# Kernel tuning notes

Measured on AMD Instinct MI355X. Metric: run time of the kernel, lower is better.

Reference implementation:

```python
import jax, jax.numpy as jnp
import numpy as np

TOPK_RATIO = 0.2
DICE_WEIGHT = 0.5
SHAPE = (2, 1, 128, 192, 192)


def setup_inputs() -> dict:
    key = jax.random.key(0)
    k1, k2 = jax.random.split(key)
    logits = jax.random.normal(k1, SHAPE, dtype=jnp.float32)
    targets = jax.random.uniform(k2, SHAPE, dtype=jnp.float32)
    return {"logits": logits, "targets": targets}


def _bce_with_logits(x, t):
    # stable: max(x,0) - x*t + log(1+exp(-|x|))
    return jnp.maximum(x, 0.0) - x * t + jnp.log1p(jnp.exp(-jnp.abs(x)))


def reference(logits, targets):
    # --- TopK BCE ---
    flat_loss = _bce_with_logits(logits, targets).reshape(-1)
    n = flat_loss.shape[0]
    k_samples = max(1, int(n * TOPK_RATIO))
    topk_losses, _ = jax.lax.top_k(flat_loss, k_samples)
    bce = jnp.mean(topk_losses)

    # --- Soft Dice ---
    p = jax.nn.sigmoid(logits).reshape(-1)
    t = targets.reshape(-1)
    intersection = jnp.sum(p * t)
    union = jnp.sum(p) + jnp.sum(t)
    dice = (2.0 * intersection + 1e-06) / (union + 1e-06)
    dice_loss = 1.0 - dice

    return bce + DICE_WEIGHT * dice_loss
```

## Files before the change

### kernel.cpp

```cpp
#include <hip/hip_runtime.h>
#include <math.h>
#include <limits.h>

#define NB1 8192
#define NB2 4096
#define VEC 4
#define NREP 4

__device__ unsigned g_H1[NB1];
__device__ unsigned g_hist2[NREP * NB2];
__device__ float    g_band[2];
__device__ unsigned g_done1 = 0;

__device__ __forceinline__ void elem_f(float x, float t, float& l, float& p) {
    float e = __expf(-fabsf(x));
    l = fmaxf(x, 0.f) - x * t + __logf(1.f + e);
    float r = __builtin_amdgcn_rcpf(1.f + e);
    p = (x >= 0.f) ? r : e * r;
}

__global__ __launch_bounds__(256) void sample_band_kernel(
    const float4* __restrict__ x4, const float4* __restrict__ t4,
    int n4, long long ks, long long M)
{
    __shared__ unsigned lh[NB1];
    __shared__ int is_last;
    for (int i = threadIdx.x; i < NB1; i += 256) lh[i] = 0u;
    __syncthreads();

    int nth = gridDim.x * 256;
    int tid = blockIdx.x * 256 + threadIdx.x;
    int S4 = n4 >> 4;
    int i0 = tid, i1 = tid + nth;

    float4 xa, ta, xb, tb;
    bool v0 = i0 < S4, v1 = i1 < S4;
    if (v0) {
        int f4 = ((i0 >> 6) << 10) + (i0 & 63);
        xa = x4[f4]; ta = t4[f4];
    }
    if (v1) {
        int f4 = ((i1 >> 6) << 10) + (i1 & 63);
        xb = x4[f4]; tb = t4[f4];
    }
    if (v0) {
        float xs[4] = {xa.x, xa.y, xa.z, xa.w};
        float ts[4] = {ta.x, ta.y, ta.z, ta.w};
        #pragma unroll
        for (int c = 0; c < 4; ++c) {
            float l, p; elem_f(xs[c], ts[c], l, p);
            atomicAdd(&lh[__float_as_uint(l) >> 19], 1u);
        }
    }
    if (v1) {
        float xs[4] = {xb.x, xb.y, xb.z, xb.w};
        float ts[4] = {tb.x, tb.y, tb.z, tb.w};
        #pragma unroll
        for (int c = 0; c < 4; ++c) {
            float l, p; elem_f(xs[c], ts[c], l, p);
            atomicAdd(&lh[__float_as_uint(l) >> 19], 1u);
        }
    }
    __syncthreads();
    for (int i = threadIdx.x; i < NB1; i += 256) {
        unsigned c = lh[i];
        if (c) atomicAdd(&g_H1[i], c);
    }
    __syncthreads();

    if (threadIdx.x == 0) {
        __threadfence();
        is_last = (atomicAdd(&g_done1, 1u) == (unsigned)(gridDim.x - 1));
    }
    __syncthreads();
    if (!is_last) return;
    __threadfence();

    const uint4* hv = (const uint4*)g_H1;
    uint4* lv = (uint4*)lh;
    for (int i = threadIdx.x; i < NB1 / 4; i += 256) lv[i] = hv[i];
    __syncthreads();
    for (int i = threadIdx.x; i < NB1; i += 256) g_H1[i] = 0u;
    if (threadIdx.x == 0) g_done1 = 0u;

    if (threadIdx.x < 64) {
        int lane = threadIdx.x;
        int base = lane << 7;
        unsigned long long chunk = 0;
        for (int j = 0; j < 128; ++j) chunk += lh[base + j];
        unsigned long long s = chunk;
        #pragma unroll
        for (int off = 1; off < 64; off <<= 1) {
            unsigned long long v = __shfl_down(s, off);
            if (lane + off < 64) s += v;
        }
        unsigned long long above = s - chunk;

        int my_bhi = INT_MAX, my_blo = -1;
        unsigned long long c = above;
        for (int j = 127; j >= 0; --j) {
            unsigned h = lh[base + j];
            if ((long long)(c + h) < ks - M) my_bhi = base + j;
            if ((long long)c > ks + M && my_blo < 0) my_blo = base + j;
            c += h;
        }
        #pragma unroll
        for (int off = 32; off; off >>= 1) {
            int a = __shfl_down(my_bhi, off); my_bhi = min(my_bhi, a);
            int b = __shfl_down(my_blo, off); my_blo = max(my_blo, b);
        }
        if (lane == 0) {
            int bhi = (my_bhi == INT_MAX) ? (NB1 - 1) : my_bhi;
            int blo = my_blo;
            float vhi = __uint_as_float((unsigned)bhi << 19);
            float vlo = (blo < 0) ? 0.f : __uint_as_float((unsigned)(blo + 1) << 19);
            if (!(vlo < vhi)) vlo = 0.f;
            g_band[0] = vlo;
            g_band[1] = vhi;
        }
    }
}

__device__ __forceinline__ void process4(
    float4 xv, float4 tv, float vlo, float vhi, float scale,
    float& sp, float& spt, float& st, float& sgt, unsigned& cnt,
    unsigned (&lhist)[NB2])
{
    float xs[4] = {xv.x, xv.y, xv.z, xv.w};
    float ts[4] = {tv.x, tv.y, tv.z, tv.w};
    #pragma unroll
    for (int c = 0; c < 4; ++c) {
        float l, p;
        elem_f(xs[c], ts[c], l, p);
        sp += p; spt += p * ts[c]; st += ts[c];
        if (l >= vhi) { cnt++; sgt += l; }
        else if (l >= vlo) {
            int b = min((int)((l - vlo) * scale), NB2 - 1);
            atomicAdd(&lhist[b], 1u);
        }
    }
}

__global__ __launch_bounds__(256, 4) void main_kernel(
    const float4* __restrict__ x4, const float4* __restrict__ t4,
    float* __restrict__ q0, float* __restrict__ q1,
    float* __restrict__ q2, float* __restrict__ q3, unsigned* __restrict__ qc,
    const float* __restrict__ xg, const float* __restrict__ tg,
    int n, int n4)
{
    __shared__ unsigned lhist[NB2];
    for (int i = threadIdx.x; i < NB2; i += 256) lhist[i] = 0u;
    __syncthreads();

    float vlo = g_band[0], vhi = g_band[1];
    float scale = (float)NB2 / (vhi - vlo);

    int base = blockIdx.x * (256 * VEC) + threadIdx.x;
    float sp = 0.f, spt = 0.f, st = 0.f, sgt = 0.f;
    unsigned cnt = 0;

    bool full = (blockIdx.x + 1) * (256 * VEC) <= n4;
    if (full) {
        float4 xv[VEC], tv[VEC];
        #pragma unroll
        for (int j = 0; j < VEC; ++j) xv[j] = x4[base + j * 256];
        #pragma unroll
        for (int j = 0; j < VEC; ++j) tv[j] = t4[base + j * 256];
        #pragma unroll
        for (int j = 0; j < VEC; ++j)
            process4(xv[j], tv[j], vlo, vhi, scale, sp, spt, st, sgt, cnt, lhist);
    } else {
        for (int j = 0; j < VEC; ++j) {
            int idx = base + j * 256;
            if (idx < n4)
                process4(x4[idx], t4[idx], vlo, vhi, scale, sp, spt, st, sgt, cnt, lhist);
        }
    }
    int tail0 = n4 << 2;
    if (blockIdx.x == 0 && threadIdx.x < (n - tail0)) {
        float x = xg[tail0 + threadIdx.x], t = tg[tail0 + threadIdx.x];
        float l, p;
        elem_f(x, t, l, p);
        sp += p; spt += p * t; st += t;
        if (l >= vhi) { cnt++; sgt += l; }
        else if (l >= vlo) {
            int b = min((int)((l - vlo) * scale), NB2 - 1);
            atomicAdd(&lhist[b], 1u);
        }
    }

    __syncthreads();
    {
        unsigned* dst = &g_hist2[(blockIdx.x & (NREP - 1)) * NB2];
        for (int i = threadIdx.x; i < NB2; i += 256) {
            unsigned c = lhist[i];
            if (c) atomicAdd(&dst[i], c);
        }
    }

    #pragma unroll
    for (int off = 32; off; off >>= 1) {
        sp  += __shfl_down(sp,  off);
        spt += __shfl_down(spt, off);
        st  += __shfl_down(st,  off);
        sgt += __shfl_down(sgt, off);
        cnt += __shfl_down(cnt, off);
    }
    __shared__ float    rs[4][4];
    __shared__ unsigned rc[4];
    int w = threadIdx.x >> 6;
    if ((threadIdx.x & 63) == 0) {
        rs[w][0] = sp; rs[w][1] = spt; rs[w][2] = st; rs[w][3] = sgt; rc[w] = cnt;
    }
    __syncthreads();
    if (threadIdx.x == 0) {
        float a0 = 0, a1 = 0, a2 = 0, a3 = 0;
        unsigned c = 0;
        #pragma unroll
        for (int i = 0; i < 4; ++i) {
            a0 += rs[i][0]; a1 += rs[i][1]; a2 += rs[i][2]; a3 += rs[i][3]; c += rc[i];
        }
        q0[blockIdx.x] = a0; q1[blockIdx.x] = a1; q2[blockIdx.x] = a2;
        q3[blockIdx.x] = a3; qc[blockIdx.x] = c;
    }
}

__global__ __launch_bounds__(1024) void final_kernel(
    const float* __restrict__ q0, const float* __restrict__ q1,
    const float* __restrict__ q2, const float* __restrict__ q3,
    const unsigned* __restrict__ qc, int nblocks,
    float* __restrict__ out, long long k)
{
    __shared__ unsigned lh[NB2];
    __shared__ double red[16][5];
    __shared__ double fin[5];

    for (int i = threadIdx.x; i < NB2; i += 1024) {
        unsigned s = 0;
        #pragma unroll
        for (int r = 0; r < NREP; ++r) {
            s += g_hist2[r * NB2 + i];
            g_hist2[r * NB2 + i] = 0u;
        }
        lh[i] = s;
    }

    double a0 = 0, a1 = 0, a2 = 0, a3 = 0, a4 = 0;
    for (int i = threadIdx.x; i < nblocks; i += 1024) {
        a0 += (double)q0[i]; a1 += (double)q1[i]; a2 += (double)q2[i];
        a3 += (double)q3[i]; a4 += (double)qc[i];
    }
    #pragma unroll
    for (int off = 32; off; off >>= 1) {
        a0 += __shfl_down(a0, off); a1 += __shfl_down(a1, off);
        a2 += __shfl_down(a2, off); a3 += __shfl_down(a3, off);
        a4 += __shfl_down(a4, off);
    }
    int w = threadIdx.x >> 6;
    if ((threadIdx.x & 63) == 0) {
        red[w][0] = a0; red[w][1] = a1; red[w][2] = a2; red[w][3] = a3; red[w][4] = a4;
    }
    __syncthreads();
    if (threadIdx.x == 0) {
        double f0 = 0, f1 = 0, f2 = 0, f3 = 0, f4 = 0;
        for (int i = 0; i < 16; ++i) {
            f0 += red[i][0]; f1 += red[i][1]; f2 += red[i][2];
            f3 += red[i][3]; f4 += red[i][4];
        }
        fin[0] = f0; fin[1] = f1; fin[2] = f2; fin[3] = f3; fin[4] = f4;
    }
    __syncthreads();
    if (threadIdx.x >= 64) return;

    int lane = threadIdx.x;
    double SP = fin[0], SPT = fin[1], ST = fin[2], SGT = fin[3];
    long long CNT = (long long)fin[4];

    double vlo = (double)g_band[0], vhi = (double)g_band[1];
    double binw = (vhi - vlo) / NB2;
    long long k2 = k - CNT;

    int base = lane << 6;
    unsigned long long cchunk = 0;
    double wchunk = 0.0;
    for (int j = 0; j < 64; ++j) {
        unsigned h = lh[base + j];
        cchunk += h;
        wchunk += (double)h * (vlo + (base + j + 0.5) * binw);
    }
    unsigned long long cs = cchunk;
    double wsum = wchunk;
    #pragma unroll
    for (int off = 1; off < 64; off <<= 1) {
        unsigned long long cv = __shfl_down(cs, off);
        double wv = __shfl_down(wsum, off);
        if (lane + off < 64) { cs += cv; wsum += wv; }
    }
    unsigned long long total = __shfl(cs, 0);
    double wtotal = __shfl(wsum, 0);

    double I = SPT, U = SP + ST;
    double dice_part = 0.5 * (1.0 - (2.0 * I + 1e-6) / (U + 1e-6));

    if (k2 <= 0) {
        if (lane == 0) out[0] = (float)(SGT / (double)k + dice_part);
        return;
    }
    if ((unsigned long long)k2 > total) {
        if (lane == 0) {
            double sum_top = SGT + wtotal + (double)(k2 - (long long)total) * vlo;
            out[0] = (float)(sum_top / (double)k + dice_part);
        }
        return;
    }
    unsigned long long c = cs - cchunk;
    double wacc = wsum - wchunk;
    for (int j = 63; j >= 0; --j) {
        unsigned h = lh[base + j];
        double val = vlo + (base + j + 0.5) * binw;
        if (c < (unsigned long long)k2 && (unsigned long long)k2 <= c + h) {
            double sum_top = SGT + wacc + (double)((long long)k2 - (long long)c) * val;
            out[0] = (float)(sum_top / (double)k + dice_part);
        }
        c += h;
        wacc += (double)h * val;
    }
}

extern "C" void kernel_launch(void* const* d_in, const int* in_sizes, int n_in,
                              void* d_out, int out_size, void* d_ws, size_t ws_size,
                              hipStream_t stream)
{
    const float* x = (const float*)d_in[0];
    const float* t = (const float*)d_in[1];
    float* out = (float*)d_out;
    int n = in_sizes[0];
    int n4 = n >> 2;
    long long k = (long long)((double)n * 0.2);
    if (k < 1) k = 1;

    long long S = (long long)(n4 >> 4) * 4;
    long long ks = (S > 0) ? (long long)((double)k * (double)S / (double)n) : 0;
    long long M = 4096;

    int tilesz = 256 * VEC;
    int grid = (n4 + tilesz - 1) / tilesz;
    if (grid < 1) grid = 1;

    int S4 = n4 >> 4;
    int sgrid = (S4 + 511) / 512;
    if (sgrid < 1) sgrid = 1;

    unsigned char* ws = (unsigned char*)d_ws;
    size_t pstride = (((size_t)grid * 4) + 255) & ~(size_t)255;
    float*    q0 = (float*)(ws);
    float*    q1 = (float*)(ws + pstride);
    float*    q2 = (float*)(ws + 2 * pstride);
    float*    q3 = (float*)(ws + 3 * pstride);
    unsigned* qc = (unsigned*)(ws + 4 * pstride);

    sample_band_kernel<<<sgrid, 256, 0, stream>>>((const float4*)x, (const float4*)t,
                                                  n4, ks, M);
    main_kernel<<<grid, 256, 0, stream>>>((const float4*)x, (const float4*)t,
                                          q0, q1, q2, q3, qc, x, t, n, n4);
    final_kernel<<<1, 1024, 0, stream>>>(q0, q1, q2, q3, qc, grid, out, k);
}
```

Baseline: 137.6 us.

## Make main kernel persistent with double-buffered async global-to-LDS loads

Replaces the one-tile-per-block main kernel with a fixed grid of 512 persistent blocks. Each wave loops over 256-float4 chunks and prefetches the next chunk into double-buffered LDS using global_load_lds while it computes the current one. The aim is to overlap memory latency with compute and to cut down block launches and histogram merges, since only 512 blocks now flush their local histograms. In exchange it uses much more LDS per block, lowers the occupancy hint to 2 and relies on hand-written vmcnt waits.

```diff
diff --git a/kernel.cpp b/kernel.cpp
--- a/kernel.cpp
+++ b/kernel.cpp
@@ -4,8 +4,8 @@
 
 #define NB1 8192
 #define NB2 4096
-#define VEC 4
 #define NREP 4
+#define GRID_MAIN 512
 
 __device__ unsigned g_H1[NB1];
 __device__ unsigned g_hist2[NREP * NB2];
@@ -17,6 +17,12 @@
     l = fmaxf(x, 0.f) - x * t + __logf(1.f + e);
     float r = __builtin_amdgcn_rcpf(1.f + e);
     p = (x >= 0.f) ? r : e * r;
+}
+
+typedef __attribute__((address_space(3))) unsigned       lds_u32;
+typedef __attribute__((address_space(1))) const unsigned glb_u32;
+__device__ __forceinline__ void gload16(const void* g, void* l) {
+    __builtin_amdgcn_global_load_lds((glb_u32*)g, (lds_u32*)l, 16, 0, 0);
 }
 
 __global__ __launch_bounds__(256) void sample_band_kernel(
@@ -121,33 +127,15 @@
     }
 }
 
-__device__ __forceinline__ void process4(
-    float4 xv, float4 tv, float vlo, float vhi, float scale,
-    float& sp, float& spt, float& st, float& sgt, unsigned& cnt,
-    unsigned (&lhist)[NB2])
-{
-    float xs[4] = {xv.x, xv.y, xv.z, xv.w};
-    float ts[4] = {tv.x, tv.y, tv.z, tv.w};
-    #pragma unroll
-    for (int c = 0; c < 4; ++c) {
-        float l, p;
-        elem_f(xs[c], ts[c], l, p);
-        sp += p; spt += p * ts[c]; st += ts[c];
-        if (l >= vhi) { cnt++; sgt += l; }
-        else if (l >= vlo) {
-            int b = min((int)((l - vlo) * scale), NB2 - 1);
-            atomicAdd(&lhist[b], 1u);
-        }
-    }
-}
-
-__global__ __launch_bounds__(256, 4) void main_kernel(
+__global__ __launch_bounds__(256, 2) void main_kernel(
     const float4* __restrict__ x4, const float4* __restrict__ t4,
     float* __restrict__ q0, float* __restrict__ q1,
     float* __restrict__ q2, float* __restrict__ q3, unsigned* __restrict__ qc,
     const float* __restrict__ xg, const float* __restrict__ tg,
     int n, int n4)
 {
+    __shared__ float4 sx[4][2][256];
+    __shared__ float4 sy[4][2][256];
     __shared__ unsigned lhist[NB2];
     for (int i = threadIdx.x; i < NB2; i += 256) lhist[i] = 0u;
     __syncthreads();
@@ -155,30 +143,94 @@
     float vlo = g_band[0], vhi = g_band[1];
     float scale = (float)NB2 / (vhi - vlo);
 
-    int base = blockIdx.x * (256 * VEC) + threadIdx.x;
+    int tid = threadIdx.x;
+    int lane = tid & 63;
+    int w = __builtin_amdgcn_readfirstlane(tid >> 6);
+
+    int nwaves = gridDim.x * 4;
+    int wid = blockIdx.x * 4 + (tid >> 6);
+    int fullChunks = n4 >> 8;
+
     float sp = 0.f, spt = 0.f, st = 0.f, sgt = 0.f;
     unsigned cnt = 0;
 
-    bool full = (blockIdx.x + 1) * (256 * VEC) <= n4;
-    if (full) {
-        float4 xv[VEC], tv[VEC];
-        #pragma unroll
-        for (int j = 0; j < VEC; ++j) xv[j] = x4[base + j * 256];
-        #pragma unroll
-        for (int j = 0; j < VEC; ++j) tv[j] = t4[base + j * 256];
-        #pragma unroll
-        for (int j = 0; j < VEC; ++j)
-            process4(xv[j], tv[j], vlo, vhi, scale, sp, spt, st, sgt, cnt, lhist);
-    } else {
-        for (int j = 0; j < VEC; ++j) {
-            int idx = base + j * 256;
-            if (idx < n4)
-                process4(x4[idx], t4[idx], vlo, vhi, scale, sp, spt, st, sgt, cnt, lhist);
-        }
-    }
+#define STAGE(c) do { \
+        int _p = (c) & 1; \
+        const float4* _gx = x4 + ((long long)(c) << 8) + lane; \
+        const float4* _gt = t4 + ((long long)(c) << 8) + lane; \
+        _Pragma("unroll") \
+        for (int _i = 0; _i < 4; ++_i) { \
+            gload16(_gx + _i * 64, &sx[w][_p][_i * 64]); \
+            gload16(_gt + _i * 64, &sy[w][_p][_i * 64]); \
+        } \
+    } while (0)
+
+#define COMPUTE(c) do { \
+        int _p = (c) & 1; \
+        _Pragma("unroll") \
+        for (int _j = 0; _j < 4; ++_j) { \
+            float4 _xv = sx[w][_p][lane + _j * 64]; \
+            float4 _tv = sy[w][_p][lane + _j * 64]; \
+            float _xs[4] = {_xv.x, _xv.y, _xv.z, _xv.w}; \
+            float _ts[4] = {_tv.x, _tv.y, _tv.z, _tv.w}; \
+            _Pragma("unroll") \
+            for (int _c = 0; _c < 4; ++_c) { \
+                float _l, _pp; \
+                elem_f(_xs[_c], _ts[_c], _l, _pp); \
+                sp += _pp; spt += _pp * _ts[_c]; st += _ts[_c]; \
+                if (_l >= vhi) { cnt++; sgt += _l; } \
+                else if (_l >= vlo) { \
+                    int _bn = min((int)((_l - vlo) * scale), NB2 - 1); \
+                    atomicAdd(&lhist[_bn], 1u); \
+                } \
+            } \
+        } \
+    } while (0)
+
+    int c = wid;
+    if (c < fullChunks) {
+        STAGE(c);
+        while (true) {
+            int cn = c + nwaves;
+            if (cn < fullChunks) {
+                STAGE(cn);
+                asm volatile("s_waitcnt vmcnt(8)" ::: "memory");
+                COMPUTE(c);
+                c = cn;
+            } else {
+                asm volatile("s_waitcnt vmcnt(0)" ::: "memory");
+                COMPUTE(c);
+                break;
+            }
+        }
+    }
+
+    if ((n4 & 255) != 0 && wid == (fullChunks % nwaves)) {
+        int base = (fullChunks << 8) + lane;
+        for (int j = 0; j < 4; ++j) {
+            int idx = base + j * 64;
+            if (idx < n4) {
+                float4 xv = x4[idx], tv = t4[idx];
+                float xs[4] = {xv.x, xv.y, xv.z, xv.w};
+                float ts[4] = {tv.x, tv.y, tv.z, tv.w};
+                #pragma unroll
+                for (int cc = 0; cc < 4; ++cc) {
+                    float l, p;
+                    elem_f(xs[cc], ts[cc], l, p);
+                    sp += p; spt += p * ts[cc]; st += ts[cc];
+                    if (l >= vhi) { cnt++; sgt += l; }
+                    else if (l >= vlo) {
+                        int b = min((int)((l - vlo) * scale), NB2 - 1);
+                        atomicAdd(&lhist[b], 1u);
+                    }
+                }
+            }
+        }
+    }
+
     int tail0 = n4 << 2;
-    if (blockIdx.x == 0 && threadIdx.x < (n - tail0)) {
-        float x = xg[tail0 + threadIdx.x], t = tg[tail0 + threadIdx.x];
+    if (blockIdx.x == 0 && tid < (n - tail0)) {
+        float x = xg[tail0 + tid], t = tg[tail0 + tid];
         float l, p;
         elem_f(x, t, l, p);
         sp += p; spt += p * t; st += t;
@@ -192,9 +244,9 @@
     __syncthreads();
     {
         unsigned* dst = &g_hist2[(blockIdx.x & (NREP - 1)) * NB2];
-        for (int i = threadIdx.x; i < NB2; i += 256) {
-            unsigned c = lhist[i];
-            if (c) atomicAdd(&dst[i], c);
+        for (int i = tid; i < NB2; i += 256) {
+            unsigned cc = lhist[i];
+            if (cc) atomicAdd(&dst[i], cc);
         }
     }
 
@@ -208,21 +260,22 @@
     }
     __shared__ float    rs[4][4];
     __shared__ unsigned rc[4];
-    int w = threadIdx.x >> 6;
-    if ((threadIdx.x & 63) == 0) {
+    if ((tid & 63) == 0) {
         rs[w][0] = sp; rs[w][1] = spt; rs[w][2] = st; rs[w][3] = sgt; rc[w] = cnt;
     }
     __syncthreads();
-    if (threadIdx.x == 0) {
+    if (tid == 0) {
         float a0 = 0, a1 = 0, a2 = 0, a3 = 0;
-        unsigned c = 0;
+        unsigned cc = 0;
         #pragma unroll
         for (int i = 0; i < 4; ++i) {
-            a0 += rs[i][0]; a1 += rs[i][1]; a2 += rs[i][2]; a3 += rs[i][3]; c += rc[i];
+            a0 += rs[i][0]; a1 += rs[i][1]; a2 += rs[i][2]; a3 += rs[i][3]; cc += rc[i];
         }
         q0[blockIdx.x] = a0; q1[blockIdx.x] = a1; q2[blockIdx.x] = a2;
-        q3[blockIdx.x] = a3; qc[blockIdx.x] = c;
-    }
+        q3[blockIdx.x] = a3; qc[blockIdx.x] = cc;
+    }
+#undef STAGE
+#undef COMPUTE
 }
 
 __global__ __launch_bounds__(1024) void final_kernel(
@@ -343,16 +396,12 @@
     long long ks = (S > 0) ? (long long)((double)k * (double)S / (double)n) : 0;
     long long M = 4096;
 
-    int tilesz = 256 * VEC;
-    int grid = (n4 + tilesz - 1) / tilesz;
-    if (grid < 1) grid = 1;
-
     int S4 = n4 >> 4;
     int sgrid = (S4 + 511) / 512;
     if (sgrid < 1) sgrid = 1;
 
     unsigned char* ws = (unsigned char*)d_ws;
-    size_t pstride = (((size_t)grid * 4) + 255) & ~(size_t)255;
+    size_t pstride = (((size_t)GRID_MAIN * 4) + 255) & ~(size_t)255;
     float*    q0 = (float*)(ws);
     float*    q1 = (float*)(ws + pstride);
     float*    q2 = (float*)(ws + 2 * pstride);
@@ -361,7 +410,7 @@
 
     sample_band_kernel<<<sgrid, 256, 0, stream>>>((const float4*)x, (const float4*)t,
                                                   n4, ks, M);
-    main_kernel<<<grid, 256, 0, stream>>>((const float4*)x, (const float4*)t,
-                                          q0, q1, q2, q3, qc, x, t, n, n4);
-    final_kernel<<<1, 1024, 0, stream>>>(q0, q1, q2, q3, qc, grid, out, k);
-}
+    main_kernel<<<GRID_MAIN, 256, 0, stream>>>((const float4*)x, (const float4*)t,
+                                               q0, q1, q2, q3, qc, x, t, n, n4);
+    final_kernel<<<1, 1024, 0, stream>>>(q0, q1, q2, q3, qc, GRID_MAIN, out, k);
+}
```

Result: slower. 148.4 us (+7.9%).

## Use fixed persistent-style main grid and finer offset coarse histogram

Applied to the files above, without the earlier changes.

The main kernel now launches a fixed 2048 blocks, each looping over a contiguous chunk instead of one 1024-float4 tile per block. This cuts the number of per-block shared-histogram flushes and partial-sum writes. The sample kernel's coarse histogram moves to 2048 bins over an offset exponent range with finer (>>17) resolution, aiming for a tighter band and fewer elements in the fine histogram. In exchange, the per-thread loop no longer batches its loads up front, so fewer loads are in flight per thread.

```diff
diff --git a/kernel.cpp b/kernel.cpp
--- a/kernel.cpp
+++ b/kernel.cpp
@@ -2,10 +2,11 @@
 #include <math.h>
 #include <limits.h>
 
-#define NB1 8192
+#define NB1 2048
+#define OFF1 6656
 #define NB2 4096
-#define VEC 4
 #define NREP 4
+#define GRID_MAIN 2048
 
 __device__ unsigned g_H1[NB1];
 __device__ unsigned g_hist2[NREP * NB2];
@@ -17,6 +18,11 @@
     l = fmaxf(x, 0.f) - x * t + __logf(1.f + e);
     float r = __builtin_amdgcn_rcpf(1.f + e);
     p = (x >= 0.f) ? r : e * r;
+}
+
+__device__ __forceinline__ int coarse_bin(float l) {
+    int b = (int)(__float_as_uint(l) >> 17) - OFF1;
+    return min(max(b, 0), NB1 - 1);
 }
 
 __global__ __launch_bounds__(256) void sample_band_kernel(
@@ -49,7 +55,7 @@
         #pragma unroll
         for (int c = 0; c < 4; ++c) {
             float l, p; elem_f(xs[c], ts[c], l, p);
-            atomicAdd(&lh[__float_as_uint(l) >> 19], 1u);
+            atomicAdd(&lh[coarse_bin(l)], 1u);
         }
     }
     if (v1) {
@@ -58,7 +64,7 @@
         #pragma unroll
         for (int c = 0; c < 4; ++c) {
             float l, p; elem_f(xs[c], ts[c], l, p);
-            atomicAdd(&lh[__float_as_uint(l) >> 19], 1u);
+            atomicAdd(&lh[coarse_bin(l)], 1u);
         }
     }
     __syncthreads();
@@ -85,9 +91,9 @@
 
     if (threadIdx.x < 64) {
         int lane = threadIdx.x;
-        int base = lane << 7;
+        int base = lane << 5;
         unsigned long long chunk = 0;
-        for (int j = 0; j < 128; ++j) chunk += lh[base + j];
+        for (int j = 0; j < 32; ++j) chunk += lh[base + j];
         unsigned long long s = chunk;
         #pragma unroll
         for (int off = 1; off < 64; off <<= 1) {
@@ -98,7 +104,7 @@
 
         int my_bhi = INT_MAX, my_blo = -1;
         unsigned long long c = above;
-        for (int j = 127; j >= 0; --j) {
+        for (int j = 31; j >= 0; --j) {
             unsigned h = lh[base + j];
             if ((long long)(c + h) < ks - M) my_bhi = base + j;
             if ((long long)c > ks + M && my_blo < 0) my_blo = base + j;
@@ -112,8 +118,9 @@
         if (lane == 0) {
             int bhi = (my_bhi == INT_MAX) ? (NB1 - 1) : my_bhi;
             int blo = my_blo;
-            float vhi = __uint_as_float((unsigned)bhi << 19);
-            float vlo = (blo < 0) ? 0.f : __uint_as_float((unsigned)(blo + 1) << 19);
+            float vhi = __uint_as_float((unsigned)(bhi + OFF1) << 17);
+            float vlo = (blo < 0) ? 0.f
+                                  : __uint_as_float((unsigned)(blo + 1 + OFF1) << 17);
             if (!(vlo < vhi)) vlo = 0.f;
             g_band[0] = vlo;
             g_band[1] = vhi;
@@ -121,27 +128,7 @@
     }
 }
 
-__device__ __forceinline__ void process4(
-    float4 xv, float4 tv, float vlo, float vhi, float scale,
-    float& sp, float& spt, float& st, float& sgt, unsigned& cnt,
-    unsigned (&lhist)[NB2])
-{
-    float xs[4] = {xv.x, xv.y, xv.z, xv.w};
-    float ts[4] = {tv.x, tv.y, tv.z, tv.w};
-    #pragma unroll
-    for (int c = 0; c < 4; ++c) {
-        float l, p;
-        elem_f(xs[c], ts[c], l, p);
-        sp += p; spt += p * ts[c]; st += ts[c];
-        if (l >= vhi) { cnt++; sgt += l; }
-        else if (l >= vlo) {
-            int b = min((int)((l - vlo) * scale), NB2 - 1);
-            atomicAdd(&lhist[b], 1u);
-        }
-    }
-}
-
-__global__ __launch_bounds__(256, 4) void main_kernel(
+__global__ __launch_bounds__(256) void main_kernel(
     const float4* __restrict__ x4, const float4* __restrict__ t4,
     float* __restrict__ q0, float* __restrict__ q1,
     float* __restrict__ q2, float* __restrict__ q3, unsigned* __restrict__ qc,
@@ -155,27 +142,30 @@
     float vlo = g_band[0], vhi = g_band[1];
     float scale = (float)NB2 / (vhi - vlo);
 
-    int base = blockIdx.x * (256 * VEC) + threadIdx.x;
+    int per = (n4 + GRID_MAIN - 1) / GRID_MAIN;
+    int base = blockIdx.x * per;
+    int end = min(base + per, n4);
+
     float sp = 0.f, spt = 0.f, st = 0.f, sgt = 0.f;
     unsigned cnt = 0;
 
-    bool full = (blockIdx.x + 1) * (256 * VEC) <= n4;
-    if (full) {
-        float4 xv[VEC], tv[VEC];
-        #pragma unroll
-        for (int j = 0; j < VEC; ++j) xv[j] = x4[base + j * 256];
-        #pragma unroll
-        for (int j = 0; j < VEC; ++j) tv[j] = t4[base + j * 256];
-        #pragma unroll
-        for (int j = 0; j < VEC; ++j)
-            process4(xv[j], tv[j], vlo, vhi, scale, sp, spt, st, sgt, cnt, lhist);
-    } else {
-        for (int j = 0; j < VEC; ++j) {
-            int idx = base + j * 256;
-            if (idx < n4)
-                process4(x4[idx], t4[idx], vlo, vhi, scale, sp, spt, st, sgt, cnt, lhist);
-        }
-    }
+    for (int idx = base + threadIdx.x; idx < end; idx += 256) {
+        float4 xv = x4[idx], tv = t4[idx];
+        float xs[4] = {xv.x, xv.y, xv.z, xv.w};
+        float ts[4] = {tv.x, tv.y, tv.z, tv.w};
+        #pragma unroll
+        for (int c = 0; c < 4; ++c) {
+            float l, p;
+            elem_f(xs[c], ts[c], l, p);
+            sp += p; spt += p * ts[c]; st += ts[c];
+            if (l >= vhi) { cnt++; sgt += l; }
+            else if (l >= vlo) {
+                int b = min((int)((l - vlo) * scale), NB2 - 1);
+                atomicAdd(&lhist[b], 1u);
+            }
+        }
+    }
+
     int tail0 = n4 << 2;
     if (blockIdx.x == 0 && threadIdx.x < (n - tail0)) {
         float x = xg[tail0 + threadIdx.x], t = tg[tail0 + threadIdx.x];
@@ -343,16 +333,12 @@
     long long ks = (S > 0) ? (long long)((double)k * (double)S / (double)n) : 0;
     long long M = 4096;
 
-    int tilesz = 256 * VEC;
-    int grid = (n4 + tilesz - 1) / tilesz;
-    if (grid < 1) grid = 1;
-
     int S4 = n4 >> 4;
     int sgrid = (S4 + 511) / 512;
     if (sgrid < 1) sgrid = 1;
 
     unsigned char* ws = (unsigned char*)d_ws;
-    size_t pstride = (((size_t)grid * 4) + 255) & ~(size_t)255;
+    size_t pstride = (((size_t)GRID_MAIN * 4) + 255) & ~(size_t)255;
     float*    q0 = (float*)(ws);
     float*    q1 = (float*)(ws + pstride);
     float*    q2 = (float*)(ws + 2 * pstride);
@@ -361,7 +347,7 @@
 
     sample_band_kernel<<<sgrid, 256, 0, stream>>>((const float4*)x, (const float4*)t,
                                                   n4, ks, M);
-    main_kernel<<<grid, 256, 0, stream>>>((const float4*)x, (const float4*)t,
-                                          q0, q1, q2, q3, qc, x, t, n, n4);
-    final_kernel<<<1, 1024, 0, stream>>>(q0, q1, q2, q3, qc, grid, out, k);
-}
+    main_kernel<<<GRID_MAIN, 256, 0, stream>>>((const float4*)x, (const float4*)t,
+                                               q0, q1, q2, q3, qc, x, t, n, n4);
+    final_kernel<<<1, 1024, 0, stream>>>(q0, q1, q2, q3, qc, GRID_MAIN, out, k);
+}
```

Measured after the change: 132.5 us (median of 2 runs). 1.04x faster.
